# Kernel optimization log

Measured on AMD Instinct MI355X. Metric: run time of the kernel, lower is better.

## Reference

```python
import jax, jax.numpy as jnp
import numpy as np

N_NODES, N_EDGES, B = 16384, 262144, 128
FEAT, HEADS, OUT_DIM, EMBED, PROT_LEN, VOCAB = 78, 10, 128, 128, 1000, 26
NEG_SLOPE = 0.2


def _gat_conv(x, src, dst, W, a_src, a_dst, b, heads, out_c):
    """PyG-style GATConv (concat heads), eval mode (no dropout)."""
    n = x.shape[0]
    xl = (x @ W).reshape(n, heads, out_c)                    # [N,H,C]
    alpha_s = jnp.einsum('nhc,hc->nh', xl, a_src)            # [N,H]
    alpha_d = jnp.einsum('nhc,hc->nh', xl, a_dst)
    e = jax.nn.leaky_relu(alpha_s[src] + alpha_d[dst], NEG_SLOPE)  # [E,H]
    # scatter-softmax over destination neighborhoods
    m = jax.ops.segment_max(e, dst, num_segments=n)
    m = jnp.where(jnp.isfinite(m), m, 0.0)
    p = jnp.exp(e - m[dst])
    s = jax.ops.segment_sum(p, dst, num_segments=n)
    alpha = p / (s[dst] + 1e-16)                             # [E,H]
    out = jax.ops.segment_sum(alpha[:, :, None] * xl[src], dst, num_segments=n)
    return out.reshape(n, heads * out_c) + b


def setup_inputs() -> dict:
    key = jax.random.key(0)
    ks = jax.random.split(key, 24)
    inp = {}
    inp['x'] = jax.random.normal(ks[0], (N_NODES, FEAT), jnp.float32)
    inp['edge_index'] = jax.random.randint(ks[1], (2, N_EDGES), 0, N_NODES)
    inp['batch'] = jnp.sort(jax.random.randint(ks[2], (N_NODES,), 0, B))
    inp['target'] = jax.random.randint(ks[3], (B, PROT_LEN), 0, VOCAB)
    s = 0.05
    rn = lambda k, sh: jax.random.normal(k, sh, jnp.float32) * s
    inp['W1'] = rn(ks[4], (FEAT, HEADS * FEAT))
    inp['att_src1'] = rn(ks[5], (HEADS, FEAT))
    inp['att_dst1'] = rn(ks[6], (HEADS, FEAT))
    inp['b1'] = jnp.zeros((HEADS * FEAT,), jnp.float32)
    # GAT layer 2: 780 -> 128, 1 head
    inp['W2'] = rn(ks[7], (HEADS * FEAT, OUT_DIM))
    inp['att_src2'] = rn(ks[8], (1, OUT_DIM))
    inp['att_dst2'] = rn(ks[9], (1, OUT_DIM))
    inp['b2'] = jnp.zeros((OUT_DIM,), jnp.float32)
    inp['fc_g1_w'] = rn(ks[10], (OUT_DIM, OUT_DIM)); inp['fc_g1_b'] = jnp.zeros((OUT_DIM,), jnp.float32)
    inp['emb'] = rn(ks[11], (VOCAB, EMBED))
    inp['conv_w'] = rn(ks[12], (32, PROT_LEN, 8)); inp['conv_b'] = jnp.zeros((32,), jnp.float32)
    inp['fc_xt_w'] = rn(ks[13], (32 * 121, OUT_DIM)); inp['fc_xt_b'] = jnp.zeros((OUT_DIM,), jnp.float32)
    inp['fc1_w'] = rn(ks[14], (256, 1024)); inp['fc1_b'] = jnp.zeros((1024,), jnp.float32)
    inp['fc2_w'] = rn(ks[15], (1024, 256)); inp['fc2_b'] = jnp.zeros((256,), jnp.float32)
    inp['out_w'] = rn(ks[16], (256, 1)); inp['out_b'] = jnp.zeros((1,), jnp.float32)
    return inp


def reference(x, edge_index, batch, target, W1, att_src1, att_dst1, b1,
              W2, att_src2, att_dst2, b2, fc_g1_w, fc_g1_b, emb, conv_w, conv_b,
              fc_xt_w, fc_xt_b, fc1_w, fc1_b, fc2_w, fc2_b, out_w, out_b):
    n = x.shape[0]
    # add self-loops (PyG GATConv default)
    loops = jnp.arange(n, dtype=edge_index.dtype)
    src = jnp.concatenate([edge_index[0], loops])
    dst = jnp.concatenate([edge_index[1], loops])
    # drug graph branch (eval: dropout = identity)
    h = jax.nn.elu(_gat_conv(x, src, dst, W1, att_src1, att_dst1, b1, HEADS, FEAT))
    h = _gat_conv(h, src, dst, W2, att_src2, att_dst2, b2, 1, OUT_DIM)
    h = jax.nn.relu(h)
    # global max pool per graph
    g = jax.ops.segment_max(h, batch, num_segments=B)
    g = jnp.where(jnp.isfinite(g), g, 0.0)
    g = jax.nn.relu(g @ fc_g1_w + fc_g1_b)                   # [B,128]
    # protein branch: embedding -> conv1d over embed axis (channels = seq pos)
    e = emb[target]                                          # [B,1000,128]
    c = jax.lax.conv_general_dilated(e, conv_w, (1,), 'VALID',
                                     dimension_numbers=('NCH', 'OIH', 'NCH'))
    c = jax.nn.relu(c + conv_b[None, :, None])               # [B,32,121]
    xt = c.reshape(-1, 32 * 121) @ fc_xt_w + fc_xt_b         # [B,128]
    # fused head
    xc = jnp.concatenate([g, xt], axis=1)                    # [B,256]
    xc = jax.nn.relu(xc @ fc1_w + fc1_b)
    xc = jax.nn.relu(xc @ fc2_w + fc2_b)
    return xc @ out_w + out_b                                # [B,1]
```

## Files before the change

### kernel.cpp

```cpp
#include <hip/hip_runtime.h>
#include <hip/hip_bf16.h>

using bf16 = __hip_bfloat16;

#define NN 16384
#define NE 262144
#define ET (NE + NN)
#define NB 128
#define FEAT 78
#define HEADS 10
#define D1 780
#define OD 128
#define PL 1000
#define VOC 26
#define SLOPE 0.2f

typedef __attribute__((ext_vector_type(8))) short short8;
typedef __attribute__((ext_vector_type(4))) float f32x4;

static __device__ __forceinline__ ushort f2bf(float f){
    bf16 h = __float2bfloat16(f);
    return *reinterpret_cast<ushort*>(&h);
}

__global__ void k_hist(const int* __restrict__ ei, int* __restrict__ cnt){
    int e = blockIdx.x*256 + threadIdx.x;
    if (e >= ET) return;
    int dst = (e < NE) ? ei[NE + e] : (e - NE);
    atomicAdd(&cnt[dst], 1);
}

__global__ __launch_bounds__(1024) void k_scan(const int* __restrict__ cnt, int* __restrict__ off){
    __shared__ int ps[1024];
    int t = threadIdx.x;
    int loc[16]; int s = 0;
#pragma unroll
    for (int j = 0; j < 16; ++j){ loc[j] = cnt[t*16 + j]; s += loc[j]; }
    ps[t] = s; __syncthreads();
    for (int d = 1; d < 1024; d <<= 1){
        int v = (t >= d) ? ps[t - d] : 0;
        __syncthreads();
        ps[t] += v;
        __syncthreads();
    }
    int run = (t == 0) ? 0 : ps[t - 1];
#pragma unroll
    for (int j = 0; j < 16; ++j){ off[t*16 + j] = run; run += loc[j]; }
    if (t == 1023) off[NN] = run;
}

__global__ void k_fill(const int* __restrict__ ei, const int* __restrict__ off,
                       int* __restrict__ cur, int* __restrict__ csrc){
    int e = blockIdx.x*256 + threadIdx.x;
    if (e >= ET) return;
    int src, dst;
    if (e < NE){ src = ei[e]; dst = ei[NE + e]; } else { src = e - NE; dst = src; }
    int p = off[dst] + atomicAdd(&cur[dst], 1);
    csrc[p] = src;
}

__global__ __launch_bounds__(256) void k_alpha1x(const float* __restrict__ x, const float* __restrict__ W1,
                                                 const float* __restrict__ asw, const float* __restrict__ adw,
                                                 float* __restrict__ as1, float* __restrict__ ad1){
    __shared__ float xs[64*79];
    __shared__ float va[D1], vd[D1];
    int n0 = blockIdx.x * 64, t = threadIdx.x;
    for (int i = t; i < 64*FEAT; i += 256){
        int n = i / FEAT, k = i % FEAT;
        xs[n*79 + k] = x[(size_t)n0*FEAT + i];
    }
    for (int idx = t; idx < D1; idx += 256){
        int h = idx / FEAT, k = idx % FEAT;
        const float* wr = W1 + (size_t)k*D1 + h*FEAT;
        const float* pa = asw + h*FEAT;
        const float* pd = adw + h*FEAT;
        float a = 0.f, d = 0.f;
        for (int j = 0; j < FEAT; ++j){ float w = wr[j]; a += w*pa[j]; d += w*pd[j]; }
        va[idx] = a; vd[idx] = d;
    }
    __syncthreads();
    for (int p = t; p < 64*HEADS; p += 256){
        int h = p >> 6, nl = p & 63;
        const float* xr = xs + nl*79;
        const float* pa = va + h*FEAT; const float* pd = vd + h*FEAT;
        float a = 0.f, d = 0.f;
        for (int k = 0; k < FEAT; ++k){ float xv = xr[k]; a += xv*pa[k]; d += xv*pd[k]; }
        as1[(size_t)(n0 + nl)*HEADS + h] = a;
        ad1[(size_t)(n0 + nl)*HEADS + h] = d;
    }
}

__global__ __launch_bounds__(64) void k_gat1x(const float* __restrict__ x, const float* __restrict__ as1,
                                              const float* __restrict__ ad1, const int* __restrict__ off,
                                              const int* __restrict__ csrc,
                                              float* __restrict__ agg){
    int dst = blockIdx.x, lane = threadIdx.x;
    int beg = off[dst], end = off[dst + 1];
    int deg = end - beg;
    float adh[HEADS];
#pragma unroll
    for (int h = 0; h < HEADS; ++h) adh[h] = ad1[(size_t)dst*HEADS + h];
    int s0 = 0;
    float p[HEADS], mx[HEADS];
#pragma unroll
    for (int h = 0; h < HEADS; ++h){ mx[h] = -1e30f; p[h] = 0.f; }
    if (lane < deg){
        s0 = csrc[beg + lane];
#pragma unroll
        for (int h = 0; h < HEADS; ++h){
            float v = as1[(size_t)s0*HEADS + h] + adh[h];
            v = v > 0.f ? v : SLOPE*v;
            p[h] = v; mx[h] = v;
        }
    }
    if (deg > 64){
        for (int e = beg + 64 + lane; e < end; e += 64){
            int s = csrc[e];
#pragma unroll
            for (int h = 0; h < HEADS; ++h){
                float v = as1[(size_t)s*HEADS + h] + adh[h];
                v = v > 0.f ? v : SLOPE*v;
                mx[h] = fmaxf(mx[h], v);
            }
        }
    }
#pragma unroll
    for (int h = 0; h < HEADS; ++h)
        for (int o = 32; o; o >>= 1) mx[h] = fmaxf(mx[h], __shfl_xor(mx[h], o));
    float sm[HEADS];
#pragma unroll
    for (int h = 0; h < HEADS; ++h) sm[h] = 0.f;
    if (lane < deg){
#pragma unroll
        for (int h = 0; h < HEADS; ++h){ p[h] = __expf(p[h] - mx[h]); sm[h] = p[h]; }
    }
    if (deg > 64){
        for (int e = beg + 64 + lane; e < end; e += 64){
            int s = csrc[e];
#pragma unroll
            for (int h = 0; h < HEADS; ++h){
                float v = as1[(size_t)s*HEADS + h] + adh[h];
                v = v > 0.f ? v : SLOPE*v;
                sm[h] += __expf(v - mx[h]);
            }
        }
    }
    float inv[HEADS];
#pragma unroll
    for (int h = 0; h < HEADS; ++h){
        for (int o = 32; o; o >>= 1) sm[h] += __shfl_xor(sm[h], o);
        inv[h] = 1.f/(sm[h] + 1e-16f);
        p[h] = (lane < deg) ? p[h]*inv[h] : 0.f;
    }
    float acc1[HEADS], acc2[HEADS];
#pragma unroll
    for (int h = 0; h < HEADS; ++h){ acc1[h] = 0.f; acc2[h] = 0.f; }
    int cnt0 = deg < 64 ? deg : 64;
    for (int c0 = 0; c0 < cnt0; c0 += 16){
        float r1[16], r2[16];
#pragma unroll
        for (int i = 0; i < 16; ++i){
            int s = __shfl(s0, c0 + i);
            const float* xr = x + (size_t)s*FEAT;
            r1[i] = xr[lane];
            r2[i] = (lane < FEAT - 64) ? xr[64 + lane] : 0.f;
        }
#pragma unroll
        for (int i = 0; i < 16; ++i){
            if (c0 + i < cnt0){
#pragma unroll
                for (int h = 0; h < HEADS; ++h){
                    float al = __shfl(p[h], c0 + i);
                    acc1[h] += al*r1[i];
                    acc2[h] += al*r2[i];
                }
            }
        }
    }
    if (deg > 64){
        for (int base = beg + 64; base < end; base += 64){
            int cnt = min(64, end - base);
            int s1 = 0;
            float pp[HEADS];
#pragma unroll
            for (int h = 0; h < HEADS; ++h) pp[h] = 0.f;
            if (lane < cnt){
                s1 = csrc[base + lane];
#pragma unroll
                for (int h = 0; h < HEADS; ++h){
                    float v = as1[(size_t)s1*HEADS + h] + adh[h];
                    v = v > 0.f ? v : SLOPE*v;
                    pp[h] = __expf(v - mx[h])*inv[h];
                }
            }
            for (int c0 = 0; c0 < cnt; c0 += 16){
                float r1[16], r2[16];
#pragma unroll
                for (int i = 0; i < 16; ++i){
                    int s = __shfl(s1, c0 + i);
                    const float* xr = x + (size_t)s*FEAT;
                    r1[i] = xr[lane];
                    r2[i] = (lane < FEAT - 64) ? xr[64 + lane] : 0.f;
                }
#pragma unroll
                for (int i = 0; i < 16; ++i){
                    if (c0 + i < cnt){
#pragma unroll
                        for (int h = 0; h < HEADS; ++h){
                            float al = __shfl(pp[h], c0 + i);
                            acc1[h] += al*r1[i];
                            acc2[h] += al*r2[i];
                        }
                    }
                }
            }
        }
    }
#pragma unroll
    for (int h = 0; h < HEADS; ++h)
        agg[(size_t)dst*D1 + h*FEAT + lane] = acc1[h];
    if (lane < FEAT - 64){
#pragma unroll
        for (int h = 0; h < HEADS; ++h)
            agg[(size_t)dst*D1 + h*FEAT + 64 + lane] = acc2[h];
    }
}

__global__ __launch_bounds__(256) void k_post1(const float* __restrict__ agg, const float* __restrict__ W1,
                                               const float* __restrict__ b1, ushort* __restrict__ h1h){
    __shared__ float w1s[FEAT][80];
    __shared__ float ags[64][81];
    __shared__ float bsh[FEAT];
    int ht = blockIdx.x >> 8;
    int nt = blockIdx.x & 255;
    int n0 = nt * 64;
    int t = threadIdx.x;
    for (int i = t; i < FEAT*FEAT; i += 256){
        int k = i / FEAT, j = i % FEAT;
        w1s[k][j] = W1[(size_t)k*D1 + ht*FEAT + j];
    }
    for (int i = t; i < 64*FEAT; i += 256){
        int r = i / FEAT, k = i % FEAT;
        ags[r][k] = agg[(size_t)(n0 + r)*D1 + ht*FEAT + k];
    }
    if (t < FEAT) bsh[t] = b1[ht*FEAT + t];
    __syncthreads();
    if (t < 208){
        int rg = t / 13, cg = t % 13;
        int c0 = cg*6;
        float acc[4][6];
#pragma unroll
        for (int i = 0; i < 4; ++i)
#pragma unroll
            for (int j = 0; j < 6; ++j) acc[i][j] = 0.f;
        for (int k = 0; k < FEAT; ++k){
            float av[4];
#pragma unroll
            for (int i = 0; i < 4; ++i) av[i] = ags[rg*4 + i][k];
            float2 w01 = *(const float2*)&w1s[k][c0];
            float2 w23 = *(const float2*)&w1s[k][c0 + 2];
            float2 w45 = *(const float2*)&w1s[k][c0 + 4];
            float wv[6] = {w01.x, w01.y, w23.x, w23.y, w45.x, w45.y};
#pragma unroll
            for (int i = 0; i < 4; ++i)
#pragma unroll
                for (int j = 0; j < 6; ++j) acc[i][j] += av[i]*wv[j];
        }
#pragma unroll
        for (int i = 0; i < 4; ++i){
#pragma unroll
            for (int j = 0; j < 6; ++j){
                float v = acc[i][j] + bsh[c0 + j];
                v = v > 0.f ? v : __expf(v) - 1.f;
                h1h[(size_t)(n0 + rg*4 + i)*D1 + ht*FEAT + c0 + j] = f2bf(v);
            }
        }
    }
}

__global__ __launch_bounds__(256) void k_w2h(const float* __restrict__ w2, ushort* __restrict__ w2h){
    int i = blockIdx.x*256 + threadIdx.x;
    w2h[i] = f2bf(w2[i]);
}

__global__ __launch_bounds__(256) void k_gemm2m(const ushort* __restrict__ h1h, const ushort* __restrict__ w2h,
                                                const float* __restrict__ s2w, const float* __restrict__ d2w,
                                                float* __restrict__ xl2,
                                                float* __restrict__ as2, float* __restrict__ ad2){
    __shared__ ushort As[64][40];
    __shared__ ushort Bs[128][40];
    int r0 = blockIdx.x * 64;
    int t = threadIdx.x;
    int w = t >> 6, l = t & 63;
    f32x4 acc[8];
#pragma unroll
    for (int i = 0; i < 8; ++i) acc[i] = (f32x4){0.f, 0.f, 0.f, 0.f};
    for (int k0 = 0; k0 < D1; k0 += 32){
        {
            int r = t >> 2, kq = (t & 3)*8;
            int gk = k0 + kq;
            ushort tmp[8];
            if (gk + 8 <= D1){
                *(ushort4*)&tmp[0] = *(const ushort4*)&h1h[(size_t)(r0 + r)*D1 + gk];
                *(ushort4*)&tmp[4] = *(const ushort4*)&h1h[(size_t)(r0 + r)*D1 + gk + 4];
            } else {
#pragma unroll
                for (int j = 0; j < 8; ++j)
                    tmp[j] = (gk + j < D1) ? h1h[(size_t)(r0 + r)*D1 + gk + j] : (ushort)0;
            }
            *(ushort4*)&As[r][kq]     = *(ushort4*)&tmp[0];
            *(ushort4*)&As[r][kq + 4] = *(ushort4*)&tmp[4];
        }
        {
            int n8 = (t & 15)*8, kk = t >> 4;
#pragma unroll
            for (int half = 0; half < 2; ++half){
                int k = kk + half*16;
                ushort tmp[8];
                if (k0 + k < D1){
                    *(uint4*)&tmp[0] = *(const uint4*)&w2h[(size_t)(k0 + k)*OD + n8];
                } else {
#pragma unroll
                    for (int j = 0; j < 8; ++j) tmp[j] = 0;
                }
#pragma unroll
                for (int j = 0; j < 8; ++j) Bs[n8 + j][k] = tmp[j];
            }
        }
        __syncthreads();
        short8 a = *(const short8*)&As[w*16 + (l & 15)][(l >> 4)*8];
#pragma unroll
        for (int nt = 0; nt < 8; ++nt){
            short8 b = *(const short8*)&Bs[nt*16 + (l & 15)][(l >> 4)*8];
            acc[nt] = __builtin_amdgcn_mfma_f32_16x16x32_bf16(a, b, acc[nt], 0, 0, 0);
        }
        __syncthreads();
    }
    int colg = l & 15, kg = l >> 4;
    float sa[4] = {0.f,0.f,0.f,0.f}, sd[4] = {0.f,0.f,0.f,0.f};
#pragma unroll
    for (int nt = 0; nt < 8; ++nt){
        int c = nt*16 + colg;
        float wsv = s2w[c], wdv = d2w[c];
#pragma unroll
        for (int r = 0; r < 4; ++r){
            float v = acc[nt][r];
            int row = r0 + w*16 + kg*4 + r;
            xl2[(size_t)row*OD + c] = v;
            sa[r] += v*wsv; sd[r] += v*wdv;
        }
    }
#pragma unroll
    for (int r = 0; r < 4; ++r){
#pragma unroll
        for (int o = 8; o; o >>= 1){ sa[r] += __shfl_xor(sa[r], o); sd[r] += __shfl_xor(sd[r], o); }
    }
    if (colg == 0){
        int row = r0 + w*16 + kg*4;
#pragma unroll
        for (int r = 0; r < 4; ++r){ as2[row + r] = sa[r]; ad2[row + r] = sd[r]; }
    }
}

__global__ __launch_bounds__(64) void k_gat2(const float* __restrict__ xl2, const float* __restrict__ as2,
                                             const float* __restrict__ ad2, const int* __restrict__ off,
                                             const int* __restrict__ csrc, const float* __restrict__ b2,
                                             float* __restrict__ h2){
    int dst = blockIdx.x, lane = threadIdx.x;
    int beg = off[dst], end = off[dst + 1];
    int deg = end - beg;
    float ad = ad2[dst];
    int s0 = 0; float v0 = -1e30f;
    if (lane < deg){
        s0 = csrc[beg + lane];
        float v = as2[s0] + ad;
        v0 = v > 0.f ? v : SLOPE*v;
    }
    float m = v0;
    if (deg > 64){
        for (int e = beg + 64 + lane; e < end; e += 64){
            float v = as2[csrc[e]] + ad; v = v > 0.f ? v : SLOPE*v;
            m = fmaxf(m, v);
        }
    }
    for (int o = 32; o; o >>= 1) m = fmaxf(m, __shfl_xor(m, o));
    float pe = (lane < deg) ? __expf(v0 - m) : 0.f;
    float sm = pe;
    if (deg > 64){
        for (int e = beg + 64 + lane; e < end; e += 64){
            float v = as2[csrc[e]] + ad; v = v > 0.f ? v : SLOPE*v;
            sm += __expf(v - m);
        }
    }
    for (int o = 32; o; o >>= 1) sm += __shfl_xor(sm, o);
    float inv = 1.f / (sm + 1e-16f);
    float p = pe * inv;
    float a0 = 0.f, a1 = 0.f;
    int cnt0 = deg < 64 ? deg : 64;
    for (int c0 = 0; c0 < cnt0; c0 += 16){
        float r1[16], r2[16];
#pragma unroll
        for (int i = 0; i < 16; ++i){
            int s = __shfl(s0, c0 + i);
            r1[i] = xl2[(size_t)s*OD + lane];
            r2[i] = xl2[(size_t)s*OD + 64 + lane];
        }
#pragma unroll
        for (int i = 0; i < 16; ++i){
            if (c0 + i < cnt0){
                float al = __shfl(p, c0 + i);
                a0 += al*r1[i];
                a1 += al*r2[i];
            }
        }
    }
    if (deg > 64){
        for (int base = beg + 64; base < end; base += 64){
            int cnt = min(64, end - base);
            int s1 = 0; float pp = 0.f;
            if (lane < cnt){
                s1 = csrc[base + lane];
                float v = as2[s1] + ad; v = v > 0.f ? v : SLOPE*v;
                pp = __expf(v - m) * inv;
            }
            for (int c0 = 0; c0 < cnt; c0 += 16){
                float r1[16], r2[16];
#pragma unroll
                for (int i = 0; i < 16; ++i){
                    int s = __shfl(s1, c0 + i);
                    r1[i] = xl2[(size_t)s*OD + lane];
                    r2[i] = xl2[(size_t)s*OD + 64 + lane];
                }
#pragma unroll
                for (int i = 0; i < 16; ++i){
                    if (c0 + i < cnt){
                        float al = __shfl(pp, c0 + i);
                        a0 += al*r1[i];
                        a1 += al*r2[i];
                    }
                }
            }
        }
    }
    float o0 = a0 + b2[lane];      o0 = o0 > 0.f ? o0 : 0.f;
    float o1 = a1 + b2[64 + lane]; o1 = o1 > 0.f ? o1 : 0.f;
    h2[(size_t)dst*OD + lane] = o0;
    h2[(size_t)dst*OD + 64 + lane] = o1;
}

__global__ __launch_bounds__(128) void k_poolfc(const float* __restrict__ h2, const int* __restrict__ batch,
                                                const float* __restrict__ w, const float* __restrict__ bias,
                                                float* __restrict__ gfc){
    __shared__ float row[OD];
    int b = blockIdx.x, t = threadIdx.x;
    int lo = 0, hi = NN;
    while (lo < hi){ int mid = (lo + hi) >> 1; if (batch[mid] < b) lo = mid + 1; else hi = mid; }
    int s0 = lo;
    lo = s0; hi = NN;
    while (lo < hi){ int mid = (lo + hi) >> 1; if (batch[mid] < b + 1) lo = mid + 1; else hi = mid; }
    int s1 = lo;
    float mx = 0.f;
    for (int n = s0; n < s1; ++n) mx = fmaxf(mx, h2[(size_t)n*OD + t]);
    row[t] = mx;
    __syncthreads();
    float acc = 0.f;
    for (int k = 0; k < OD; ++k) acc += row[k] * w[k*OD + t];
    acc += bias[t];
    gfc[b*OD + t] = acc > 0.f ? acc : 0.f;
}

__global__ __launch_bounds__(256) void k_wt(const float* __restrict__ convw, float* __restrict__ wt){
    int idx = blockIdx.x*256 + threadIdx.x;
    int i = idx >> 8, ok = idx & 255;
    wt[idx] = convw[(size_t)(ok >> 3)*PL*8 + (size_t)i*8 + (ok & 7)];
}

__global__ __launch_bounds__(256) void k_abuild(const int* __restrict__ target, const float* __restrict__ wt,
                                                float* __restrict__ Ag){
    __shared__ int Ai[VOC][256];
    __shared__ int tss[256];
    int b = blockIdx.x >> 2, seg = blockIdx.x & 3;
    int t = threadIdx.x;
#pragma unroll
    for (int v = 0; v < VOC; ++v) Ai[v][t] = 0;
    if (t < 250) tss[t] = target[b*PL + seg*250 + t];
    __syncthreads();
    const float* wtb = wt + (size_t)(seg*250)*256 + t;
    const float SC = 16777216.0f;
    for (int i = 0; i < 250; ++i){
        float w = wtb[(size_t)i*256];
        int q = __float2int_rn(w * SC);
        atomicAdd(&Ai[tss[i]][t], q);
    }
    __syncthreads();
    const float INV = 5.9604644775390625e-08f;
    float* Ao = Ag + (size_t)blockIdx.x*VOC*256 + t;
#pragma unroll
    for (int v = 0; v < VOC; ++v) Ao[(size_t)v*256] = (float)Ai[v][t] * INV;
}

__global__ __launch_bounds__(256) void k_conv(const float* __restrict__ Ag, const float* __restrict__ emb,
                                              const float* __restrict__ convb, float* __restrict__ cbuf){
    __shared__ float As[VOC][128];
    __shared__ float embs[VOC*128 + 16];
    int b = blockIdx.x >> 1, half = blockIdx.x & 1;
    int t = threadIdx.x;
    for (int i = t; i < VOC*128; i += 256){
        int v = i >> 7, c = i & 127;
        float s = 0.f;
#pragma unroll
        for (int seg = 0; seg < 4; ++seg)
            s += Ag[((size_t)(b*4 + seg)*VOC + v)*256 + half*128 + c];
        As[v][c] = s;
        embs[i] = emb[i];
    }
    if (t < 16) embs[VOC*128 + t] = 0.f;
    __syncthreads();
    int o_l = t >> 4, pg = t & 15, p0 = pg * 8;
    float accp[8];
#pragma unroll
    for (int i = 0; i < 8; ++i) accp[i] = 0.f;
    for (int v = 0; v < VOC; ++v){
        float w[15];
        const float* er = embs + v*128 + p0;
#pragma unroll
        for (int i = 0; i < 15; ++i) w[i] = er[i];
#pragma unroll
        for (int k2 = 0; k2 < 8; ++k2){
            float a = As[v][o_l*8 + k2];
#pragma unroll
            for (int j = 0; j < 8; ++j) accp[j] += a * w[j + k2];
        }
    }
    float cbv = convb[half*16 + o_l];
#pragma unroll
    for (int j = 0; j < 8; ++j){
        int p = p0 + j;
        if (p < 121){
            float v2 = accp[j] + cbv;
            cbuf[(size_t)b*3872 + (half*16 + o_l)*121 + p] = v2 > 0.f ? v2 : 0.f;
        }
    }
}

__global__ __launch_bounds__(256) void k_xt(const float* __restrict__ cbuf, const float* __restrict__ fxw,
                                            float* __restrict__ xtp){
    __shared__ float csh[16][242];
    int kt = blockIdx.x >> 3, bt = blockIdx.x & 7;
    int t = threadIdx.x;
    for (int i = t; i < 16*242; i += 256){
        int bb = i / 242, kk = i % 242;
        csh[bb][kk] = cbuf[(size_t)(bt*16 + bb)*3872 + kt*242 + kk];
    }
    __syncthreads();
    int j = t & 127, bh = t >> 7;
    float acc[8];
#pragma unroll
    for (int i = 0; i < 8; ++i) acc[i] = 0.f;
    for (int kk = 0; kk < 242; ++kk){
        float w = fxw[(size_t)(kt*242 + kk)*128 + j];
#pragma unroll
        for (int bb = 0; bb < 8; ++bb) acc[bb] += csh[bh*8 + bb][kk] * w;
    }
#pragma unroll
    for (int bb = 0; bb < 8; ++bb)
        xtp[(size_t)kt*NB*128 + (size_t)(bt*16 + bh*8 + bb)*128 + j] = acc[bb];
}

__global__ __launch_bounds__(256) void k_fc1(const float* __restrict__ gfc, const float* __restrict__ xtp,
                                             const float* __restrict__ fxb,
                                             const float* __restrict__ w, const float* __restrict__ bias,
                                             float* __restrict__ out){
    __shared__ float xc[256];
    int b = blockIdx.x >> 2, nt = blockIdx.x & 3;
    int t = threadIdx.x;
    if (t < 128) xc[t] = gfc[b*OD + t];
    else {
        int j = t - 128;
        float s = fxb[j];
#pragma unroll
        for (int kt = 0; kt < 16; ++kt) s += xtp[(size_t)kt*NB*128 + (size_t)b*128 + j];
        xc[t] = s;
    }
    __syncthreads();
    int j = nt*256 + t;
    float acc = 0.f;
    for (int k = 0; k < 256; ++k) acc += xc[k] * w[(size_t)k*1024 + j];
    acc += bias[j];
    out[b*1024 + j] = acc > 0.f ? acc : 0.f;
}

__global__ __launch_bounds__(256) void k_fc2p(const float* __restrict__ hf1, const float* __restrict__ w,
                                              float* __restrict__ part){
    __shared__ float row[256];
    int b = blockIdx.x >> 2, ks = blockIdx.x & 3;
    int t = threadIdx.x;
    row[t] = hf1[b*1024 + ks*256 + t];
    __syncthreads();
    float acc = 0.f;
    const float* wc = w + (size_t)(ks*256)*256 + t;
    for (int k = 0; k < 256; ++k) acc += row[k] * wc[(size_t)k*256];
    part[((size_t)ks*NB + b)*256 + t] = acc;
}

__global__ __launch_bounds__(256) void k_fc2red(const float* __restrict__ part, const float* __restrict__ bias,
                                                const float* __restrict__ ow, const float* __restrict__ ob,
                                                float* __restrict__ out){
    __shared__ float s2[256];
    int b = blockIdx.x, t = threadIdx.x;
    float v = part[(size_t)b*256 + t] + part[((size_t)NB + b)*256 + t]
            + part[((size_t)2*NB + b)*256 + t] + part[((size_t)3*NB + b)*256 + t];
    v += bias[t];
    v = v > 0.f ? v : 0.f;
    s2[t] = v * ow[t];
    __syncthreads();
    if (t < 64){
        float a = s2[t] + s2[t + 64] + s2[t + 128] + s2[t + 192];
#pragma unroll
        for (int o = 32; o; o >>= 1) a += __shfl_xor(a, o);
        if (t == 0) out[b] = a + ob[0];
    }
}

extern "C" void kernel_launch(void* const* d_in, const int* in_sizes, int n_in,
                              void* d_out, int out_size, void* d_ws, size_t ws_size,
                              hipStream_t stream){
    const float* x    = (const float*)d_in[0];
    const int*  ei    = (const int*)d_in[1];
    const int*  batch = (const int*)d_in[2];
    const int*  target= (const int*)d_in[3];
    const float* W1   = (const float*)d_in[4];
    const float* as1w = (const float*)d_in[5];
    const float* ad1w = (const float*)d_in[6];
    const float* b1   = (const float*)d_in[7];
    const float* W2   = (const float*)d_in[8];
    const float* as2w = (const float*)d_in[9];
    const float* ad2w = (const float*)d_in[10];
    const float* b2   = (const float*)d_in[11];
    const float* fgw  = (const float*)d_in[12];
    const float* fgb  = (const float*)d_in[13];
    const float* emb  = (const float*)d_in[14];
    const float* cw   = (const float*)d_in[15];
    const float* cb   = (const float*)d_in[16];
    const float* fxw  = (const float*)d_in[17];
    const float* fxb  = (const float*)d_in[18];
    const float* f1w  = (const float*)d_in[19];
    const float* f1b  = (const float*)d_in[20];
    const float* f2w  = (const float*)d_in[21];
    const float* f2b  = (const float*)d_in[22];
    const float* ow   = (const float*)d_in[23];
    const float* ob   = (const float*)d_in[24];

    float* f = (float*)d_ws;
    size_t o = 0;
    float* agg = f + o; o += (size_t)NN*D1;
    float* h1f = f + o; o += (size_t)NN*D1;
    float* as1 = f + o; o += (size_t)NN*HEADS;
    float* ad1 = f + o; o += (size_t)NN*HEADS;
    float* xl2 = f + o; o += (size_t)NN*OD;
    float* h2  = f + o; o += (size_t)NN*OD;
    float* as2 = f + o; o += NN;
    float* ad2 = f + o; o += NN;
    float* gfc = f + o; o += NB*OD;
    float* hf1 = f + o; o += NB*1024;
    float* part= f + o; o += (size_t)4*NB*256;
    float* wt  = f + o; o += (size_t)PL*256;
    float* cbuf= f + o; o += (size_t)NB*3872;
    float* xtp = f + o; o += (size_t)16*NB*128;
    float* w2hf= f + o; o += (size_t)D1*OD/2 + 64;
    int* cnt   = (int*)(f + o); o += NN;
    int* off   = (int*)(f + o); o += NN + 1;
    int* csrc  = (int*)(f + o); o += ET;
    ushort* h1h = (ushort*)h1f;
    ushort* w2h = (ushort*)w2hf;
    float* Ag  = h1f;
    (void)ws_size; (void)in_sizes; (void)n_in; (void)out_size;

    hipMemsetAsync(cnt, 0, NN*sizeof(int), stream);
    k_hist<<<(ET + 255)/256, 256, 0, stream>>>(ei, cnt);
    k_scan<<<1, 1024, 0, stream>>>(cnt, off);
    hipMemsetAsync(cnt, 0, NN*sizeof(int), stream);
    k_fill<<<(ET + 255)/256, 256, 0, stream>>>(ei, off, cnt, csrc);

    k_alpha1x<<<NN/64, 256, 0, stream>>>(x, W1, as1w, ad1w, as1, ad1);
    k_gat1x<<<NN, 64, 0, stream>>>(x, as1, ad1, off, csrc, agg);
    k_post1<<<HEADS*256, 256, 0, stream>>>(agg, W1, b1, h1h);

    k_w2h<<<(D1*OD)/256, 256, 0, stream>>>(W2, w2h);
    k_gemm2m<<<NN/64, 256, 0, stream>>>(h1h, w2h, as2w, ad2w, xl2, as2, ad2);
    k_gat2<<<NN, 64, 0, stream>>>(xl2, as2, ad2, off, csrc, b2, h2);

    k_poolfc<<<NB, 128, 0, stream>>>(h2, batch, fgw, fgb, gfc);

    k_wt<<<1000, 256, 0, stream>>>(cw, wt);
    k_abuild<<<NB*4, 256, 0, stream>>>(target, wt, Ag);
    k_conv<<<NB*2, 256, 0, stream>>>(Ag, emb, cb, cbuf);
    k_xt<<<128, 256, 0, stream>>>(cbuf, fxw, xtp);

    k_fc1<<<NB*4, 256, 0, stream>>>(gfc, xtp, fxb, f1w, f1b, hf1);
    k_fc2p<<<NB*4, 256, 0, stream>>>(hf1, f2w, part);
    k_fc2red<<<NB, 256, 0, stream>>>(part, f2b, ow, ob, (float*)d_out);
}
```

Measured before the change: 408.8 us.

## Precompute per-edge attention logits in CSR order and store GAT1 aggregate as bf16

Adds a destination array to the CSR build and two new edge-parallel kernels that compute leaky-relu attention logits for every edge in CSR order. The per-destination GAT kernels then read these contiguous logits instead of gathering source scores by index several times, which is meant to replace repeated random gathers with streaming loads. The layer-1 aggregate is also written as bf16 and converted back in the post-projection kernel, halving that intermediate's traffic. The costs are two extra launches, extra writes of the edge-logit buffers, and reduced precision in the aggregate.

```diff
diff --git a/kernel.cpp b/kernel.cpp
--- a/kernel.cpp
+++ b/kernel.cpp
@@ -22,6 +22,11 @@
     bf16 h = __float2bfloat16(f);
     return *reinterpret_cast<ushort*>(&h);
 }
+static __device__ __forceinline__ float bf2f(ushort u){
+    bf16 h;
+    *reinterpret_cast<ushort*>(&h) = u;
+    return __bfloat162float(h);
+}
 
 __global__ void k_hist(const int* __restrict__ ei, int* __restrict__ cnt){
     int e = blockIdx.x*256 + threadIdx.x;
@@ -50,13 +55,14 @@
 }
 
 __global__ void k_fill(const int* __restrict__ ei, const int* __restrict__ off,
-                       int* __restrict__ cur, int* __restrict__ csrc){
+                       int* __restrict__ cur, int* __restrict__ csrc, int* __restrict__ cdst){
     int e = blockIdx.x*256 + threadIdx.x;
     if (e >= ET) return;
     int src, dst;
     if (e < NE){ src = ei[e]; dst = ei[NE + e]; } else { src = e - NE; dst = src; }
     int p = off[dst] + atomicAdd(&cur[dst], 1);
     csrc[p] = src;
+    cdst[p] = dst;
 }
 
 __global__ __launch_bounds__(256) void k_alpha1x(const float* __restrict__ x, const float* __restrict__ W1,
@@ -90,38 +96,40 @@
     }
 }
 
-__global__ __launch_bounds__(64) void k_gat1x(const float* __restrict__ x, const float* __restrict__ as1,
-                                              const float* __restrict__ ad1, const int* __restrict__ off,
-                                              const int* __restrict__ csrc,
-                                              float* __restrict__ agg){
+__global__ __launch_bounds__(256) void k_edge1(const float* __restrict__ as1, const float* __restrict__ ad1,
+                                               const int* __restrict__ csrc, const int* __restrict__ cdst,
+                                               float* __restrict__ e1){
+    int e = blockIdx.x*256 + threadIdx.x;
+    if (e >= ET) return;
+    int s = csrc[e], d = cdst[e];
+#pragma unroll
+    for (int h = 0; h < HEADS; ++h){
+        float v = as1[(size_t)s*HEADS + h] + ad1[(size_t)d*HEADS + h];
+        e1[(size_t)e*HEADS + h] = v > 0.f ? v : SLOPE*v;
+    }
+}
+
+__global__ __launch_bounds__(64) void k_gat1x(const float* __restrict__ x, const float* __restrict__ e1,
+                                              const int* __restrict__ off, const int* __restrict__ csrc,
+                                              ushort* __restrict__ aggh){
     int dst = blockIdx.x, lane = threadIdx.x;
     int beg = off[dst], end = off[dst + 1];
     int deg = end - beg;
-    float adh[HEADS];
-#pragma unroll
-    for (int h = 0; h < HEADS; ++h) adh[h] = ad1[(size_t)dst*HEADS + h];
     int s0 = 0;
     float p[HEADS], mx[HEADS];
 #pragma unroll
     for (int h = 0; h < HEADS; ++h){ mx[h] = -1e30f; p[h] = 0.f; }
     if (lane < deg){
         s0 = csrc[beg + lane];
-#pragma unroll
-        for (int h = 0; h < HEADS; ++h){
-            float v = as1[(size_t)s0*HEADS + h] + adh[h];
-            v = v > 0.f ? v : SLOPE*v;
-            p[h] = v; mx[h] = v;
-        }
+        const float* er = e1 + (size_t)(beg + lane)*HEADS;
+#pragma unroll
+        for (int h = 0; h < HEADS; ++h){ p[h] = er[h]; mx[h] = er[h]; }
     }
     if (deg > 64){
         for (int e = beg + 64 + lane; e < end; e += 64){
-            int s = csrc[e];
-#pragma unroll
-            for (int h = 0; h < HEADS; ++h){
-                float v = as1[(size_t)s*HEADS + h] + adh[h];
-                v = v > 0.f ? v : SLOPE*v;
-                mx[h] = fmaxf(mx[h], v);
-            }
+            const float* er = e1 + (size_t)e*HEADS;
+#pragma unroll
+            for (int h = 0; h < HEADS; ++h) mx[h] = fmaxf(mx[h], er[h]);
         }
     }
 #pragma unroll
@@ -136,13 +144,9 @@
     }
     if (deg > 64){
         for (int e = beg + 64 + lane; e < end; e += 64){
-            int s = csrc[e];
-#pragma unroll
-            for (int h = 0; h < HEADS; ++h){
-                float v = as1[(size_t)s*HEADS + h] + adh[h];
-                v = v > 0.f ? v : SLOPE*v;
-                sm[h] += __expf(v - mx[h]);
-            }
+            const float* er = e1 + (size_t)e*HEADS;
+#pragma unroll
+            for (int h = 0; h < HEADS; ++h) sm[h] += __expf(er[h] - mx[h]);
         }
     }
     float inv[HEADS];
@@ -186,12 +190,10 @@
             for (int h = 0; h < HEADS; ++h) pp[h] = 0.f;
             if (lane < cnt){
                 s1 = csrc[base + lane];
-#pragma unroll
-                for (int h = 0; h < HEADS; ++h){
-                    float v = as1[(size_t)s1*HEADS + h] + adh[h];
-                    v = v > 0.f ? v : SLOPE*v;
-                    pp[h] = __expf(v - mx[h])*inv[h];
-                }
+                const float* er = e1 + (size_t)(base + lane)*HEADS;
+#pragma unroll
+                for (int h = 0; h < HEADS; ++h)
+                    pp[h] = __expf(er[h] - mx[h])*inv[h];
             }
             for (int c0 = 0; c0 < cnt; c0 += 16){
                 float r1[16], r2[16];
@@ -218,15 +220,15 @@
     }
 #pragma unroll
     for (int h = 0; h < HEADS; ++h)
-        agg[(size_t)dst*D1 + h*FEAT + lane] = acc1[h];
+        aggh[(size_t)dst*D1 + h*FEAT + lane] = f2bf(acc1[h]);
     if (lane < FEAT - 64){
 #pragma unroll
         for (int h = 0; h < HEADS; ++h)
-            agg[(size_t)dst*D1 + h*FEAT + 64 + lane] = acc2[h];
-    }
-}
-
-__global__ __launch_bounds__(256) void k_post1(const float* __restrict__ agg, const float* __restrict__ W1,
+            aggh[(size_t)dst*D1 + h*FEAT + 64 + lane] = f2bf(acc2[h]);
+    }
+}
+
+__global__ __launch_bounds__(256) void k_post1(const ushort* __restrict__ aggh, const float* __restrict__ W1,
                                                const float* __restrict__ b1, ushort* __restrict__ h1h){
     __shared__ float w1s[FEAT][80];
     __shared__ float ags[64][81];
@@ -241,7 +243,7 @@
     }
     for (int i = t; i < 64*FEAT; i += 256){
         int r = i / FEAT, k = i % FEAT;
-        ags[r][k] = agg[(size_t)(n0 + r)*D1 + ht*FEAT + k];
+        ags[r][k] = bf2f(aggh[(size_t)(n0 + r)*D1 + ht*FEAT + k]);
     }
     if (t < FEAT) bsh[t] = b1[ht*FEAT + t];
     __syncthreads();
@@ -362,35 +364,37 @@
     }
 }
 
-__global__ __launch_bounds__(64) void k_gat2(const float* __restrict__ xl2, const float* __restrict__ as2,
-                                             const float* __restrict__ ad2, const int* __restrict__ off,
-                                             const int* __restrict__ csrc, const float* __restrict__ b2,
-                                             float* __restrict__ h2){
+__global__ __launch_bounds__(256) void k_edge2(const float* __restrict__ as2, const float* __restrict__ ad2,
+                                               const int* __restrict__ csrc, const int* __restrict__ cdst,
+                                               float* __restrict__ e2){
+    int e = blockIdx.x*256 + threadIdx.x;
+    if (e >= ET) return;
+    float v = as2[csrc[e]] + ad2[cdst[e]];
+    e2[e] = v > 0.f ? v : SLOPE*v;
+}
+
+__global__ __launch_bounds__(64) void k_gat2(const float* __restrict__ xl2, const float* __restrict__ e2,
+                                             const int* __restrict__ off, const int* __restrict__ csrc,
+                                             const float* __restrict__ b2, float* __restrict__ h2){
     int dst = blockIdx.x, lane = threadIdx.x;
     int beg = off[dst], end = off[dst + 1];
     int deg = end - beg;
-    float ad = ad2[dst];
     int s0 = 0; float v0 = -1e30f;
     if (lane < deg){
         s0 = csrc[beg + lane];
-        float v = as2[s0] + ad;
-        v0 = v > 0.f ? v : SLOPE*v;
+        v0 = e2[beg + lane];
     }
     float m = v0;
     if (deg > 64){
-        for (int e = beg + 64 + lane; e < end; e += 64){
-            float v = as2[csrc[e]] + ad; v = v > 0.f ? v : SLOPE*v;
-            m = fmaxf(m, v);
-        }
+        for (int e = beg + 64 + lane; e < end; e += 64)
+            m = fmaxf(m, e2[e]);
     }
     for (int o = 32; o; o >>= 1) m = fmaxf(m, __shfl_xor(m, o));
     float pe = (lane < deg) ? __expf(v0 - m) : 0.f;
     float sm = pe;
     if (deg > 64){
-        for (int e = beg + 64 + lane; e < end; e += 64){
-            float v = as2[csrc[e]] + ad; v = v > 0.f ? v : SLOPE*v;
-            sm += __expf(v - m);
-        }
+        for (int e = beg + 64 + lane; e < end; e += 64)
+            sm += __expf(e2[e] - m);
     }
     for (int o = 32; o; o >>= 1) sm += __shfl_xor(sm, o);
     float inv = 1.f / (sm + 1e-16f);
@@ -420,8 +424,7 @@
             int s1 = 0; float pp = 0.f;
             if (lane < cnt){
                 s1 = csrc[base + lane];
-                float v = as2[s1] + ad; v = v > 0.f ? v : SLOPE*v;
-                pp = __expf(v - m) * inv;
+                pp = __expf(e2[base + lane] - m) * inv;
             }
             for (int c0 = 0; c0 < cnt; c0 += 16){
                 float r1[16], r2[16];
@@ -653,7 +656,7 @@
 
     float* f = (float*)d_ws;
     size_t o = 0;
-    float* agg = f + o; o += (size_t)NN*D1;
+    float* aggf = f + o; o += (size_t)NN*D1;
     float* h1f = f + o; o += (size_t)NN*D1;
     float* as1 = f + o; o += (size_t)NN*HEADS;
     float* ad1 = f + o; o += (size_t)NN*HEADS;
@@ -668,27 +671,33 @@
     float* cbuf= f + o; o += (size_t)NB*3872;
     float* xtp = f + o; o += (size_t)16*NB*128;
     float* w2hf= f + o; o += (size_t)D1*OD/2 + 64;
+    float* e2  = f + o; o += ET;
     int* cnt   = (int*)(f + o); o += NN;
     int* off   = (int*)(f + o); o += NN + 1;
     int* csrc  = (int*)(f + o); o += ET;
-    ushort* h1h = (ushort*)h1f;
-    ushort* w2h = (ushort*)w2hf;
-    float* Ag  = h1f;
+    int* cdst  = (int*)(f + o); o += ET;
+    ushort* aggh = (ushort*)aggf;
+    float*  e1   = aggf + (size_t)NN*D1/2;
+    ushort* h1h  = (ushort*)h1f;
+    ushort* w2h  = (ushort*)w2hf;
+    float*  Ag   = h1f;
     (void)ws_size; (void)in_sizes; (void)n_in; (void)out_size;
 
     hipMemsetAsync(cnt, 0, NN*sizeof(int), stream);
     k_hist<<<(ET + 255)/256, 256, 0, stream>>>(ei, cnt);
     k_scan<<<1, 1024, 0, stream>>>(cnt, off);
     hipMemsetAsync(cnt, 0, NN*sizeof(int), stream);
-    k_fill<<<(ET + 255)/256, 256, 0, stream>>>(ei, off, cnt, csrc);
+    k_fill<<<(ET + 255)/256, 256, 0, stream>>>(ei, off, cnt, csrc, cdst);
 
     k_alpha1x<<<NN/64, 256, 0, stream>>>(x, W1, as1w, ad1w, as1, ad1);
-    k_gat1x<<<NN, 64, 0, stream>>>(x, as1, ad1, off, csrc, agg);
-    k_post1<<<HEADS*256, 256, 0, stream>>>(agg, W1, b1, h1h);
+    k_edge1<<<(ET + 255)/256, 256, 0, stream>>>(as1, ad1, csrc, cdst, e1);
+    k_gat1x<<<NN, 64, 0, stream>>>(x, e1, off, csrc, aggh);
+    k_post1<<<HEADS*256, 256, 0, stream>>>(aggh, W1, b1, h1h);
 
     k_w2h<<<(D1*OD)/256, 256, 0, stream>>>(W2, w2h);
     k_gemm2m<<<NN/64, 256, 0, stream>>>(h1h, w2h, as2w, ad2w, xl2, as2, ad2);
-    k_gat2<<<NN, 64, 0, stream>>>(xl2, as2, ad2, off, csrc, b2, h2);
+    k_edge2<<<(ET + 255)/256, 256, 0, stream>>>(as2, ad2, csrc, cdst, e2);
+    k_gat2<<<NN, 64, 0, stream>>>(xl2, e2, off, csrc, b2, h2);
 
     k_poolfc<<<NB, 128, 0, stream>>>(h2, batch, fgw, fgb, gfc);
 
```

Result: slower. 418.5 us (+2.4%).
